# Performance work log

Hardware: AMD Instinct MI355X
Metric: run time of the kernel (lower is better)

Reference implementation:

```python
import jax, jax.numpy as jnp
import numpy as np

B, NS, NF, T, D = 64, 2, 13, 24, 512
H = 8
DH = D // H
DFF = 2048
EPS = 1e-5


def setup_inputs() -> dict:
    key = jax.random.key(0)
    ks = jax.random.split(key, 16)
    s = 0.02
    inp = {
        'x': jax.random.normal(ks[0], (B, NS * NF, T, D), jnp.float32),
        'w_in_s': jax.random.normal(ks[1], (3 * D, D), jnp.float32) * s,
        'b_in_s': jnp.zeros((3 * D,), jnp.float32),
        'w_out_s': jax.random.normal(ks[2], (D, D), jnp.float32) * s,
        'b_out_s': jnp.zeros((D,), jnp.float32),
        'w_in_f': jax.random.normal(ks[3], (3 * D, D), jnp.float32) * s,
        'b_in_f': jnp.zeros((3 * D,), jnp.float32),
        'w_out_f': jax.random.normal(ks[4], (D, D), jnp.float32) * s,
        'b_out_f': jnp.zeros((D,), jnp.float32),
        'w1': jax.random.normal(ks[5], (DFF, D), jnp.float32) * s,
        'b1': jnp.zeros((DFF,), jnp.float32),
        'w2': jax.random.normal(ks[6], (D, DFF), jnp.float32) * s,
        'b2': jnp.zeros((D,), jnp.float32),
        'g1': jnp.ones((D,), jnp.float32), 'be1': jnp.zeros((D,), jnp.float32),
        'g2': jnp.ones((D,), jnp.float32), 'be2': jnp.zeros((D,), jnp.float32),
        'g3': jnp.ones((D,), jnp.float32), 'be3': jnp.zeros((D,), jnp.float32),
    }
    return inp


def _layer_norm(x, g, b):
    mu = jnp.mean(x, axis=-1, keepdims=True)
    var = jnp.mean(jnp.square(x - mu), axis=-1, keepdims=True)
    return (x - mu) * jax.lax.rsqrt(var + EPS) * g + b


def _mha(x, w_in, b_in, w_out, b_out):
    # x: [..., S, D]; torch nn.MultiheadAttention math, eval mode (no dropout)
    qkv = x @ w_in.T + b_in                     # [..., S, 3D]
    q, k, v = jnp.split(qkv, 3, axis=-1)
    shp = q.shape[:-1] + (H, DH)
    q, k, v = q.reshape(shp), k.reshape(shp), v.reshape(shp)
    scores = jnp.einsum('...qhd,...khd->...hqk', q, k) / np.sqrt(DH).astype(np.float32)
    a = jax.nn.softmax(scores, axis=-1)
    o = jnp.einsum('...hqk,...khd->...qhd', a, v).reshape(x.shape)
    return o @ w_out.T + b_out


def reference(x, w_in_s, b_in_s, w_out_s, b_out_s, w_in_f, b_in_f, w_out_f, b_out_f,
              w1, b1, w2, b2, g1, be1, g2, be2, g3, be3):
    xr = x.reshape(B, NS, NF, T, D)
    # station attention: attend over the NS axis for each (feature, t)
    xs = xr.transpose(0, 2, 3, 1, 4)            # [B, NF, T, NS, D]
    xs = xs + _mha(xs, w_in_s, b_in_s, w_out_s, b_out_s)
    x = xs.transpose(0, 3, 1, 2, 4).reshape(B, NS * NF, T, D)
    x = _layer_norm(x, g1, be1)
    # feature attention: attend over the NF axis for each (station, t)
    xr = x.reshape(B, NS, NF, T, D)
    xf = xr.transpose(0, 1, 3, 2, 4)            # [B, NS, T, NF, D]
    xf = xf + _mha(xf, w_in_f, b_in_f, w_out_f, b_out_f)
    x = xf.transpose(0, 1, 3, 2, 4).reshape(B, NS * NF, T, D)
    x = _layer_norm(x, g2, be2)
    # feed-forward
    ff = jax.nn.relu(x @ w1.T + b1) @ w2.T + b2
    x = _layer_norm(x + ff, g3, be3)
    return x
```

## Files before the change

### kernel.cpp

```cpp
#include <hip/hip_runtime.h>
#include <stdint.h>

typedef unsigned short u16;
typedef __bf16 bf16x8 __attribute__((ext_vector_type(8)));
typedef float f32x4 __attribute__((ext_vector_type(4)));

#define DEV __device__ __forceinline__

DEV float bf2f(u16 u) {
    union { uint32_t u; float f; } c; c.u = ((uint32_t)u) << 16; return c.f;
}
DEV u16 f2bf(float f) {
    union { float f; uint32_t u; } c; c.f = f;
    uint32_t u = c.u;
    u += 0x7FFFu + ((u >> 16) & 1u);
    return (u16)(u >> 16);
}

DEV void gload_lds16(const u16* gp, u16* lp) {
    __builtin_amdgcn_global_load_lds(
        (__attribute__((address_space(1))) u16*)(uintptr_t)gp,
        (__attribute__((address_space(3))) u16*)lp,
        16, 0, 0);
}

DEV void load16f(const u16* p, float* f) {
    uint4 a = *reinterpret_cast<const uint4*>(p);
    uint4 b = *reinterpret_cast<const uint4*>(p + 8);
    uint32_t w[8] = { a.x, a.y, a.z, a.w, b.x, b.y, b.z, b.w };
#pragma unroll
    for (int k = 0; k < 8; ++k) {
        union { uint32_t u; float f; } lo, hi;
        lo.u = w[k] << 16; hi.u = w[k] & 0xFFFF0000u;
        f[2 * k] = lo.f; f[2 * k + 1] = hi.f;
    }
}
DEV float dot16(const u16* p, const float* q) {
    uint4 a = *reinterpret_cast<const uint4*>(p);
    uint4 b = *reinterpret_cast<const uint4*>(p + 8);
    uint32_t w[8] = { a.x, a.y, a.z, a.w, b.x, b.y, b.z, b.w };
    float d = 0.0f;
#pragma unroll
    for (int k = 0; k < 8; ++k) {
        union { uint32_t u; float f; } lo, hi;
        lo.u = w[k] << 16; hi.u = w[k] & 0xFFFF0000u;
        d += q[2 * k] * lo.f;
        d += q[2 * k + 1] * hi.f;
    }
    return d;
}
DEV void fma16(const u16* p, float pw, float* acc) {
    uint4 a = *reinterpret_cast<const uint4*>(p);
    uint4 b = *reinterpret_cast<const uint4*>(p + 8);
    uint32_t w[8] = { a.x, a.y, a.z, a.w, b.x, b.y, b.z, b.w };
#pragma unroll
    for (int k = 0; k < 8; ++k) {
        union { uint32_t u; float f; } lo, hi;
        lo.u = w[k] << 16; hi.u = w[k] & 0xFFFF0000u;
        acc[2 * k] += pw * lo.f;
        acc[2 * k + 1] += pw * hi.f;
    }
}
DEV void store16(u16* p, const float* y) {
    uint32_t w[8];
#pragma unroll
    for (int k = 0; k < 8; ++k)
        w[k] = (uint32_t)f2bf(y[2 * k]) | ((uint32_t)f2bf(y[2 * k + 1]) << 16);
    uint4 a = { w[0], w[1], w[2], w[3] };
    uint4 b = { w[4], w[5], w[6], w[7] };
    *reinterpret_cast<uint4*>(p) = a;
    *reinterpret_cast<uint4*>(p + 8) = b;
}

__global__ __launch_bounds__(256) void k_f32_to_bf16(
    const float* __restrict__ in, u16* __restrict__ out, int n4)
{
    int i = blockIdx.x * 256 + threadIdx.x;
    if (i >= n4) return;
    float4 v = reinterpret_cast<const float4*>(in)[i];
    ushort4 o;
    o.x = f2bf(v.x); o.y = f2bf(v.y); o.z = f2bf(v.z); o.w = f2bf(v.w);
    reinterpret_cast<ushort4*>(out)[i] = o;
}

template<bool RELU, bool RESID, int NT>
__global__ __launch_bounds__(256) void k_gemm(
    const u16* __restrict__ A, const u16* __restrict__ W,
    const float* __restrict__ bias, const u16* __restrict__ res,
    u16* __restrict__ C, int M, int N, int K)
{
    __shared__ __align__(16) u16 As[128 * 32];
    __shared__ __align__(16) u16 Bs[128 * 32];

    const int tid  = threadIdx.x;
    const int lane = tid & 63;
    const int wave = tid >> 6;
    const int wm   = wave >> 1;
    const int wn   = wave & 1;

    const int bid = blockIdx.x;
    const int xcd = bid & 7;
    const int j0  = bid >> 3;
    const long tileM = (long)(xcd * 39 + j0 / NT) * 128;
    const long tileN = (long)(j0 % NT) * 128;

    f32x4 acc[4][4] = {};

    const int r4 = tid >> 2;
    const int c8 = ((tid & 3) ^ ((tid >> 3) & 3)) * 8;
    const u16* Ab = A + (tileM + r4) * (long)K + c8;
    const u16* Wb = W + (tileN + r4) * (long)K + c8;
    u16* ldsA0 = As + wave * 512;
    u16* ldsA1 = As + 2048 + wave * 512;
    u16* ldsB0 = Bs + wave * 512;
    u16* ldsB1 = Bs + 2048 + wave * 512;

    const int arow = wm * 64 + (lane & 15);
    const int brow = wn * 64 + (lane & 15);
    const int koff = ((lane >> 4) ^ ((lane >> 1) & 3)) * 8;

    for (int kk = 0; kk < K; kk += 32) {
        gload_lds16(Ab + kk,                 ldsA0);
        gload_lds16(Ab + kk + (long)64 * K,  ldsA1);
        gload_lds16(Wb + kk,                 ldsB0);
        gload_lds16(Wb + kk + (long)64 * K,  ldsB1);
        __syncthreads();

        bf16x8 a[4], b[4];
#pragma unroll
        for (int f = 0; f < 4; ++f) {
            a[f] = *reinterpret_cast<const bf16x8*>(&As[(arow + f * 16) * 32 + koff]);
            b[f] = *reinterpret_cast<const bf16x8*>(&Bs[(brow + f * 16) * 32 + koff]);
        }
#pragma unroll
        for (int i = 0; i < 4; ++i)
#pragma unroll
            for (int j = 0; j < 4; ++j)
                acc[i][j] = __builtin_amdgcn_mfma_f32_16x16x32_bf16(
                    a[i], b[j], acc[i][j], 0, 0, 0);
        __syncthreads();
    }

    const int crow = (int)tileM + wm * 64 + ((lane >> 4) << 2);
    const int ccol = (int)tileN + wn * 64 + (lane & 15);
#pragma unroll
    for (int i = 0; i < 4; ++i) {
#pragma unroll
        for (int j = 0; j < 4; ++j) {
            const int col = ccol + j * 16;
            const float bv = bias[col];
#pragma unroll
            for (int r = 0; r < 4; ++r) {
                const long row = crow + i * 16 + r;
                float v = acc[i][j][r] + bv;
                if (RESID) v += bf2f(res[row * N + col]);
                if (RELU)  v = fmaxf(v, 0.0f);
                C[row * N + col] = f2bf(v);
            }
        }
    }
}

__global__ __launch_bounds__(256) void k_attn_s(
    const u16* __restrict__ qkv, u16* __restrict__ o)
{
    const int wave = threadIdx.x >> 6, lane = threadIdx.x & 63;
    const int g = blockIdx.x * 4 + wave;
    const int t = g % 24, bf = g / 24, f = bf % 13, b = bf / 13;
    const int base = b * 624 + f * 24 + t;
    const int h = lane >> 3, i = (lane >> 2) & 1, c = lane & 3;
    const int off = h * 64 + c * 16;

    float qf[16];
    load16f(qkv + (size_t)(base + i * 312) * 1536 + off, qf);

    float s[2];
#pragma unroll
    for (int j = 0; j < 2; ++j) {
        float d = dot16(qkv + (size_t)(base + j * 312) * 1536 + 512 + off, qf);
        d += __shfl_xor(d, 1);
        d += __shfl_xor(d, 2);
        s[j] = d * 0.125f;
    }
    const float m = fmaxf(s[0], s[1]);
    const float e0 = expf(s[0] - m), e1 = expf(s[1] - m);
    const float inv = 1.0f / (e0 + e1);
    const float p0 = e0 * inv, p1 = e1 * inv;

    float acc[16] = {};
    fma16(qkv + (size_t)base * 1536 + 1024 + off, p0, acc);
    fma16(qkv + (size_t)(base + 312) * 1536 + 1024 + off, p1, acc);

    store16(o + (size_t)(base + i * 312) * 512 + off, acc);
}

__global__ __launch_bounds__(256) void k_attn_f(
    const u16* __restrict__ qkv, u16* __restrict__ o)
{
    const int wave = threadIdx.x >> 6, lane = threadIdx.x & 63;
    const int p = blockIdx.x * 4 + wave;
    const int h = p & 7, g = p >> 3;
    const int t = g % 24, bs = g / 24, st = bs % 2, b = bs / 2;
    const int base = b * 624 + st * 312 + t;
    const int i = lane >> 2, c = lane & 3;
    const int iq = (i < 13) ? i : 12;
    const int off = h * 64 + c * 16;

    float qf[16];
    load16f(qkv + (size_t)(base + iq * 24) * 1536 + off, qf);

    float sc[13];
#pragma unroll
    for (int j = 0; j < 13; ++j) {
        float d = dot16(qkv + (size_t)(base + j * 24) * 1536 + 512 + off, qf);
        d += __shfl_xor(d, 1);
        d += __shfl_xor(d, 2);
        sc[j] = d * 0.125f;
    }
    float m = sc[0];
#pragma unroll
    for (int j = 1; j < 13; ++j) m = fmaxf(m, sc[j]);
    float den = 0.0f;
#pragma unroll
    for (int j = 0; j < 13; ++j) { sc[j] = expf(sc[j] - m); den += sc[j]; }
    const float inv = 1.0f / den;

    float acc[16] = {};
#pragma unroll
    for (int j = 0; j < 13; ++j)
        fma16(qkv + (size_t)(base + j * 24) * 1536 + 1024 + off, sc[j], acc);
#pragma unroll
    for (int e = 0; e < 16; ++e) acc[e] *= inv;

    if (i < 13)
        store16(o + (size_t)(base + i * 24) * 512 + off, acc);
}

template<bool OUTF32>
__global__ __launch_bounds__(256) void k_ln(
    const u16* __restrict__ in, const float* __restrict__ g,
    const float* __restrict__ be, u16* __restrict__ outb,
    float* __restrict__ outf)
{
    const int row  = blockIdx.x * 4 + (threadIdx.x >> 6);
    const int lane = threadIdx.x & 63;
    const u16* p = in + (size_t)row * 512 + lane * 8;

    uint4 va = *reinterpret_cast<const uint4*>(p);
    uint32_t ua[4] = { va.x, va.y, va.z, va.w };
    float x[8];
#pragma unroll
    for (int i = 0; i < 4; ++i) {
        x[2 * i]     = bf2f((u16)(ua[i] & 0xFFFFu));
        x[2 * i + 1] = bf2f((u16)(ua[i] >> 16));
    }
    float s = 0.f, sq = 0.f;
#pragma unroll
    for (int i = 0; i < 8; ++i) { s += x[i]; sq += x[i] * x[i]; }
#pragma unroll
    for (int off = 32; off; off >>= 1) {
        s  += __shfl_xor(s, off);
        sq += __shfl_xor(sq, off);
    }
    const float mean = s * (1.0f / 512.0f);
    const float var  = sq * (1.0f / 512.0f) - mean * mean;
    const float rstd = rsqrtf(var + 1e-5f);

    const int col = lane * 8;
    float4 g0 = *reinterpret_cast<const float4*>(g + col);
    float4 g1 = *reinterpret_cast<const float4*>(g + col + 4);
    float4 b0 = *reinterpret_cast<const float4*>(be + col);
    float4 b1 = *reinterpret_cast<const float4*>(be + col + 4);
    float gg[8] = { g0.x, g0.y, g0.z, g0.w, g1.x, g1.y, g1.z, g1.w };
    float bb[8] = { b0.x, b0.y, b0.z, b0.w, b1.x, b1.y, b1.z, b1.w };

    float y[8];
#pragma unroll
    for (int i = 0; i < 8; ++i) y[i] = (x[i] - mean) * rstd * gg[i] + bb[i];

    if (OUTF32) {
        float4 o0 = { y[0], y[1], y[2], y[3] };
        float4 o1 = { y[4], y[5], y[6], y[7] };
        reinterpret_cast<float4*>(outf + (size_t)row * 512 + col)[0] = o0;
        reinterpret_cast<float4*>(outf + (size_t)row * 512 + col + 4)[0] = o1;
    } else {
        uint32_t w[4];
#pragma unroll
        for (int i = 0; i < 4; ++i)
            w[i] = (uint32_t)f2bf(y[2 * i]) | ((uint32_t)f2bf(y[2 * i + 1]) << 16);
        uint4 ov = { w[0], w[1], w[2], w[3] };
        *reinterpret_cast<uint4*>(outb + (size_t)row * 512 + col) = ov;
    }
}

extern "C" void kernel_launch(void* const* d_in, const int* in_sizes, int n_in,
                              void* d_out, int out_size, void* d_ws, size_t ws_size,
                              hipStream_t stream)
{
    const float* x       = (const float*)d_in[0];
    const float* w_in_s  = (const float*)d_in[1];
    const float* b_in_s  = (const float*)d_in[2];
    const float* w_out_s = (const float*)d_in[3];
    const float* b_out_s = (const float*)d_in[4];
    const float* w_in_f  = (const float*)d_in[5];
    const float* b_in_f  = (const float*)d_in[6];
    const float* w_out_f = (const float*)d_in[7];
    const float* b_out_f = (const float*)d_in[8];
    const float* w1      = (const float*)d_in[9];
    const float* b1      = (const float*)d_in[10];
    const float* w2      = (const float*)d_in[11];
    const float* b2      = (const float*)d_in[12];
    const float* g1      = (const float*)d_in[13];
    const float* be1     = (const float*)d_in[14];
    const float* g2      = (const float*)d_in[15];
    const float* be2     = (const float*)d_in[16];
    const float* g3      = (const float*)d_in[17];
    const float* be3     = (const float*)d_in[18];

    const int R = 39936;
    u16* xb   = (u16*)d_ws;
    u16* buf1 = xb + (size_t)R * 512;
    u16* obuf = buf1 + (size_t)R * 1536;
    u16* wqs  = buf1 + (size_t)R * 2048;
    u16* wos  = wqs + 1536 * 512;
    u16* wqf  = wos + 512 * 512;
    u16* wof  = wqf + 1536 * 512;
    u16* w1b  = wof + 512 * 512;
    u16* w2b  = w1b + 2048 * 512;

    auto conv = [&](const float* src, u16* dst, int n) {
        int n4 = n / 4;
        k_f32_to_bf16<<<dim3((n4 + 255) / 256), dim3(256), 0, stream>>>(src, dst, n4);
    };
    conv(x,       xb,  R * 512);
    conv(w_in_s,  wqs, 1536 * 512);
    conv(w_out_s, wos, 512 * 512);
    conv(w_in_f,  wqf, 1536 * 512);
    conv(w_out_f, wof, 512 * 512);
    conv(w1,      w1b, 2048 * 512);
    conv(w2,      w2b, 512 * 2048);

    const dim3 blk(256);

    k_gemm<false, false, 12><<<dim3(312 * 12), blk, 0, stream>>>(
        xb, wqs, b_in_s, nullptr, buf1, R, 1536, 512);
    k_attn_s<<<dim3(19968 / 4), blk, 0, stream>>>(buf1, obuf);
    k_gemm<false, true, 4><<<dim3(312 * 4), blk, 0, stream>>>(
        obuf, wos, b_out_s, xb, xb, R, 512, 512);
    k_ln<false><<<dim3(R / 4), blk, 0, stream>>>(xb, g1, be1, xb, nullptr);

    k_gemm<false, false, 12><<<dim3(312 * 12), blk, 0, stream>>>(
        xb, wqf, b_in_f, nullptr, buf1, R, 1536, 512);
    k_attn_f<<<dim3(24576 / 4), blk, 0, stream>>>(buf1, obuf);
    k_gemm<false, true, 4><<<dim3(312 * 4), blk, 0, stream>>>(
        obuf, wof, b_out_f, xb, xb, R, 512, 512);
    k_ln<false><<<dim3(R / 4), blk, 0, stream>>>(xb, g2, be2, xb, nullptr);

    k_gemm<true, false, 16><<<dim3(312 * 16), blk, 0, stream>>>(
        xb, w1b, b1, nullptr, buf1, R, 2048, 512);
    k_gemm<false, true, 4><<<dim3(312 * 4), blk, 0, stream>>>(
        buf1, w2b, b2, xb, xb, R, 512, 2048);
    k_ln<true><<<dim3(R / 4), blk, 0, stream>>>(xb, g3, be3, nullptr, (float*)d_out);
}
```

Measured before the change: 690.2 us.

## Rewrite GEMM as 256-row tiles with 4-stage async LDS pipeline

```diff
diff --git a/kernel.cpp b/kernel.cpp
--- a/kernel.cpp
+++ b/kernel.cpp
@@ -23,6 +23,13 @@
         (__attribute__((address_space(3))) u16*)lp,
         16, 0, 0);
 }
+
+#define WAITVM8 asm volatile("s_waitcnt vmcnt(8)" ::: "memory")
+#define WAITVM6 asm volatile("s_waitcnt vmcnt(6)" ::: "memory")
+#define WAITVM4 asm volatile("s_waitcnt vmcnt(4)" ::: "memory")
+#define WAITVM3 asm volatile("s_waitcnt vmcnt(3)" ::: "memory")
+#define WAITVM0 asm volatile("s_waitcnt vmcnt(0)" ::: "memory")
+#define LDSFENCE do { asm volatile("" ::: "memory"); __builtin_amdgcn_sched_barrier(0); } while (0)
 
 DEV void load16f(const u16* p, float* f) {
     uint4 a = *reinterpret_cast<const uint4*>(p);
@@ -83,79 +90,108 @@
     reinterpret_cast<ushort4*>(out)[i] = o;
 }
 
-template<bool RELU, bool RESID, int NT>
-__global__ __launch_bounds__(256) void k_gemm(
+template<int BN, int WM, int WN, bool RELU, bool RESID, int NT>
+__global__ __launch_bounds__(512, 2) void k_gemm256(
     const u16* __restrict__ A, const u16* __restrict__ W,
     const float* __restrict__ bias, const u16* __restrict__ res,
     u16* __restrict__ C, int M, int N, int K)
 {
-    __shared__ __align__(16) u16 As[128 * 32];
-    __shared__ __align__(16) u16 Bs[128 * 32];
+    constexpr int MR = (256 / WM) / 16;
+    constexpr int NR = (BN / WN) / 16;
+    constexpr int SLOT_B = BN * 32;
+
+    __shared__ __align__(16) u16 As[4 * 8192];
+    __shared__ __align__(16) u16 Bs[4 * SLOT_B];
 
     const int tid  = threadIdx.x;
     const int lane = tid & 63;
     const int wave = tid >> 6;
-    const int wm   = wave >> 1;
-    const int wn   = wave & 1;
-
-    const int bid = blockIdx.x;
-    const int xcd = bid & 7;
-    const int j0  = bid >> 3;
-    const long tileM = (long)(xcd * 39 + j0 / NT) * 128;
-    const long tileN = (long)(j0 % NT) * 128;
-
-    f32x4 acc[4][4] = {};
+    const int wm   = wave / WN;
+    const int wn   = wave % WN;
+    const int l15  = lane & 15;
+
+    const int nwg = gridDim.x;
+    const int v   = (blockIdx.x & 7) * (nwg >> 3) + (blockIdx.x >> 3);
+    const long tileM = (long)(v / NT) * 256;
+    const long tileN = (long)(v % NT) * BN;
+
+    const int nK = K >> 5;
+
+    f32x4 acc[MR][NR] = {};
 
     const int r4 = tid >> 2;
     const int c8 = ((tid & 3) ^ ((tid >> 3) & 3)) * 8;
-    const u16* Ab = A + (tileM + r4) * (long)K + c8;
-    const u16* Wb = W + (tileN + r4) * (long)K + c8;
-    u16* ldsA0 = As + wave * 512;
-    u16* ldsA1 = As + 2048 + wave * 512;
-    u16* ldsB0 = Bs + wave * 512;
-    u16* ldsB1 = Bs + 2048 + wave * 512;
-
-    const int arow = wm * 64 + (lane & 15);
-    const int brow = wn * 64 + (lane & 15);
+    const u16* Aq = A + (tileM + r4) * (long)K + c8;
+    const u16* Bq = W + (tileN + r4) * (long)K + c8;
+
     const int koff = ((lane >> 4) ^ ((lane >> 1) & 3)) * 8;
 
-    for (int kk = 0; kk < K; kk += 32) {
-        gload_lds16(Ab + kk,                 ldsA0);
-        gload_lds16(Ab + kk + (long)64 * K,  ldsA1);
-        gload_lds16(Wb + kk,                 ldsB0);
-        gload_lds16(Wb + kk + (long)64 * K,  ldsB1);
-        __syncthreads();
-
-        bf16x8 a[4], b[4];
-#pragma unroll
-        for (int f = 0; f < 4; ++f) {
-            a[f] = *reinterpret_cast<const bf16x8*>(&As[(arow + f * 16) * 32 + koff]);
-            b[f] = *reinterpret_cast<const bf16x8*>(&Bs[(brow + f * 16) * 32 + koff]);
-        }
-#pragma unroll
-        for (int i = 0; i < 4; ++i)
-#pragma unroll
-            for (int j = 0; j < 4; ++j)
-                acc[i][j] = __builtin_amdgcn_mfma_f32_16x16x32_bf16(
-                    a[i], b[j], acc[i][j], 0, 0, 0);
-        __syncthreads();
-    }
-
-    const int crow = (int)tileM + wm * 64 + ((lane >> 4) << 2);
-    const int ccol = (int)tileN + wn * 64 + (lane & 15);
-#pragma unroll
-    for (int i = 0; i < 4; ++i) {
-#pragma unroll
-        for (int j = 0; j < 4; ++j) {
-            const int col = ccol + j * 16;
+    auto stage = [&](int t) {
+        const int ko = t << 5;
+        u16* a0 = As + (t & 3) * 8192 + wave * 512;
+        u16* b0 = Bs + (t & 3) * SLOT_B + wave * 512;
+        gload_lds16(Aq + ko, a0);
+        gload_lds16(Aq + ko + (long)128 * K, a0 + 4096);
+        gload_lds16(Bq + ko, b0);
+        if constexpr (BN == 256)
+            gload_lds16(Bq + ko + (long)128 * K, b0 + 4096);
+    };
+    auto body = [&](int slot) {
+        const u16* ab = As + slot * 8192;
+        const u16* bb = Bs + slot * SLOT_B;
+        bf16x8 a[MR], b[NR];
+#pragma unroll
+        for (int n = 0; n < NR; ++n)
+            b[n] = *reinterpret_cast<const bf16x8*>(
+                &bb[(wn * (NR * 16) + n * 16 + l15) * 32 + koff]);
+#pragma unroll
+        for (int m = 0; m < MR; ++m)
+            a[m] = *reinterpret_cast<const bf16x8*>(
+                &ab[(wm * (MR * 16) + m * 16 + l15) * 32 + koff]);
+        __builtin_amdgcn_s_setprio(1);
+#pragma unroll
+        for (int m = 0; m < MR; ++m)
+#pragma unroll
+            for (int n = 0; n < NR; ++n)
+                acc[m][n] = __builtin_amdgcn_mfma_f32_16x16x32_bf16(
+                    a[m], b[n], acc[m][n], 0, 0, 0);
+        __builtin_amdgcn_s_setprio(0);
+    };
+
+    stage(0); stage(1); stage(2);
+
+    int t = 0;
+    for (; t < nK - 2; ++t) {
+        if constexpr (BN == 256) { WAITVM8; } else { WAITVM6; }
+        __builtin_amdgcn_s_barrier();
+        LDSFENCE;
+        if (t + 3 < nK) stage(t + 3);
+        body(t & 3);
+    }
+    if constexpr (BN == 256) { WAITVM4; } else { WAITVM3; }
+    __builtin_amdgcn_s_barrier();
+    LDSFENCE;
+    body(t & 3); ++t;
+    WAITVM0;
+    __builtin_amdgcn_s_barrier();
+    LDSFENCE;
+    body(t & 3);
+
+    const int crow = (int)tileM + wm * (MR * 16) + ((lane >> 4) << 2);
+    const int ccol = (int)tileN + wn * (NR * 16) + l15;
+#pragma unroll
+    for (int m = 0; m < MR; ++m) {
+#pragma unroll
+        for (int n = 0; n < NR; ++n) {
+            const int col = ccol + n * 16;
             const float bv = bias[col];
 #pragma unroll
             for (int r = 0; r < 4; ++r) {
-                const long row = crow + i * 16 + r;
-                float v = acc[i][j][r] + bv;
-                if (RESID) v += bf2f(res[row * N + col]);
-                if (RELU)  v = fmaxf(v, 0.0f);
-                C[row * N + col] = f2bf(v);
+                const long row = crow + m * 16 + r;
+                float vv = acc[m][n][r] + bv;
+                if (RESID) vv += bf2f(res[row * N + col]);
+                if (RELU)  vv = fmaxf(vv, 0.0f);
+                C[row * N + col] = f2bf(vv);
             }
         }
     }
@@ -340,25 +376,26 @@
     conv(w1,      w1b, 2048 * 512);
     conv(w2,      w2b, 512 * 2048);
 
-    const dim3 blk(256);
-
-    k_gemm<false, false, 12><<<dim3(312 * 12), blk, 0, stream>>>(
+    const dim3 blk256(256);
+    const dim3 blk512(512);
+
+    k_gemm256<256, 2, 4, false, false, 6><<<dim3(936), blk512, 0, stream>>>(
         xb, wqs, b_in_s, nullptr, buf1, R, 1536, 512);
-    k_attn_s<<<dim3(19968 / 4), blk, 0, stream>>>(buf1, obuf);
-    k_gemm<false, true, 4><<<dim3(312 * 4), blk, 0, stream>>>(
+    k_attn_s<<<dim3(19968 / 4), blk256, 0, stream>>>(buf1, obuf);
+    k_gemm256<128, 4, 2, false, true, 4><<<dim3(624), blk512, 0, stream>>>(
         obuf, wos, b_out_s, xb, xb, R, 512, 512);
-    k_ln<false><<<dim3(R / 4), blk, 0, stream>>>(xb, g1, be1, xb, nullptr);
-
-    k_gemm<false, false, 12><<<dim3(312 * 12), blk, 0, stream>>>(
+    k_ln<false><<<dim3(R / 4), blk256, 0, stream>>>(xb, g1, be1, xb, nullptr);
+
+    k_gemm256<256, 2, 4, false, false, 6><<<dim3(936), blk512, 0, stream>>>(
         xb, wqf, b_in_f, nullptr, buf1, R, 1536, 512);
-    k_attn_f<<<dim3(24576 / 4), blk, 0, stream>>>(buf1, obuf);
-    k_gemm<false, true, 4><<<dim3(312 * 4), blk, 0, stream>>>(
+    k_attn_f<<<dim3(24576 / 4), blk256, 0, stream>>>(buf1, obuf);
+    k_gemm256<128, 4, 2, false, true, 4><<<dim3(624), blk512, 0, stream>>>(
         obuf, wof, b_out_f, xb, xb, R, 512, 512);
-    k_ln<false><<<dim3(R / 4), blk, 0, stream>>>(xb, g2, be2, xb, nullptr);
-
-    k_gemm<true, false, 16><<<dim3(312 * 16), blk, 0, stream>>>(
+    k_ln<false><<<dim3(R / 4), blk256, 0, stream>>>(xb, g2, be2, xb, nullptr);
+
+    k_gemm256<256, 2, 4, true, false, 8><<<dim3(1248), blk512, 0, stream>>>(
         xb, w1b, b1, nullptr, buf1, R, 2048, 512);
-    k_gemm<false, true, 4><<<dim3(312 * 4), blk, 0, stream>>>(
+    k_gemm256<128, 4, 2, false, true, 4><<<dim3(624), blk512, 0, stream>>>(
         buf1, w2b, b2, xb, xb, R, 512, 2048);
-    k_ln<true><<<dim3(R / 4), blk, 0, stream>>>(xb, g3, be3, nullptr, (float*)d_out);
-}
+    k_ln<true><<<dim3(R / 4), blk256, 0, stream>>>(xb, g3, be3, nullptr, (float*)d_out);
+}
```

Measured after the change: 727.3 us. 1.05x slower.
